# Optimization experiments

Hardware: AMD Instinct MI355X
Metric: run time of the kernel (lower is better)

Reference implementation:

```python
import jax, jax.numpy as jnp
import numpy as np

N = 100000
E = 1600000
IN_C = 64
HID = 32
HEADS = 4
OUT_C = 1
NEG_SLOPE = 0.2
BN_EPS = 1e-5


def setup_inputs() -> dict:
    key = jax.random.key(0)
    ks = jax.random.split(key, 12)
    x = jax.random.normal(ks[0], (N, IN_C), dtype=jnp.float32)
    edge_index = jax.random.randint(ks[1], (2, E), 0, N, dtype=jnp.int32)
    # GATConv layer 1: in -> heads*hid, concat=True
    W1 = jax.random.normal(ks[2], (IN_C, HEADS * HID), dtype=jnp.float32) * (1.0 / np.sqrt(IN_C))
    att_src1 = jax.random.normal(ks[3], (HEADS, HID), dtype=jnp.float32) * 0.1
    att_dst1 = jax.random.normal(ks[4], (HEADS, HID), dtype=jnp.float32) * 0.1
    b1 = jnp.zeros((HEADS * HID,), dtype=jnp.float32)
    # GATConv layer 2: heads*hid -> out, heads=1, concat=False
    W2 = jax.random.normal(ks[5], (HEADS * HID, OUT_C), dtype=jnp.float32) * (1.0 / np.sqrt(HEADS * HID))
    att_src2 = jax.random.normal(ks[6], (1, OUT_C), dtype=jnp.float32) * 0.1
    att_dst2 = jax.random.normal(ks[7], (1, OUT_C), dtype=jnp.float32) * 0.1
    b2 = jnp.zeros((OUT_C,), dtype=jnp.float32)
    # BatchNorm1d (eval mode, running stats)
    bn_gamma = jnp.ones((HEADS * HID,), dtype=jnp.float32)
    bn_beta = jnp.zeros((HEADS * HID,), dtype=jnp.float32)
    bn_mean = jnp.zeros((HEADS * HID,), dtype=jnp.float32)
    bn_var = jnp.ones((HEADS * HID,), dtype=jnp.float32)
    return {"x": x, "edge_index": edge_index, "W1": W1, "att_src1": att_src1,
            "att_dst1": att_dst1, "b1": b1, "W2": W2, "att_src2": att_src2,
            "att_dst2": att_dst2, "b2": b2, "bn_gamma": bn_gamma, "bn_beta": bn_beta,
            "bn_mean": bn_mean, "bn_var": bn_var}


def _gat_layer(x, src, dst, W, a_src, a_dst, heads, out_c, n):
    # linear transform, split heads: [N, heads, out_c]
    h = (x @ W).reshape(n, heads, out_c)
    # per-node attention terms: [N, heads]
    alpha_s = jnp.einsum('nhc,hc->nh', h, a_src)
    alpha_d = jnp.einsum('nhc,hc->nh', h, a_dst)
    # edge logits: [E, heads]
    e = jax.nn.leaky_relu(alpha_s[src] + alpha_d[dst], NEG_SLOPE)
    # segment softmax over edges sharing a destination node
    e_max = jax.ops.segment_max(e, dst, num_segments=n)
    e = jnp.exp(e - e_max[dst])
    denom = jax.ops.segment_sum(e, dst, num_segments=n)
    alpha = e / (denom[dst] + 1e-16)                 # [E, heads]
    msg = h[src] * alpha[:, :, None]                 # [E, heads, out_c]
    return jax.ops.segment_sum(msg, dst, num_segments=n)  # [N, heads, out_c]


def reference(x, edge_index, W1, att_src1, att_dst1, b1, W2, att_src2, att_dst2,
              b2, bn_gamma, bn_beta, bn_mean, bn_var):
    n = x.shape[0]
    loops = jnp.arange(n, dtype=edge_index.dtype)
    src = jnp.concatenate([edge_index[0], loops])    # PyG GATConv adds self-loops
    dst = jnp.concatenate([edge_index[1], loops])
    # layer 1: concat heads
    h = _gat_layer(x, src, dst, W1, att_src1, att_dst1, HEADS, HID, n)
    h = h.reshape(n, HEADS * HID) + b1
    # BatchNorm1d (eval) + ELU (dropout is identity in eval)
    h = (h - bn_mean) * jax.lax.rsqrt(bn_var + BN_EPS) * bn_gamma + bn_beta
    h = jax.nn.elu(h)
    # layer 2: single head, concat=False (mean over 1 head == squeeze)
    out = _gat_layer(h, src, dst, W2, att_src2, att_dst2, 1, OUT_C, n)
    return out.reshape(n, OUT_C) + b2
```

## Files before the change

### kernel.cpp

```cpp
#include <hip/hip_runtime.h>
#include <cstdint>
#include <cstddef>

#define NEG_SLOPE 0.2f
#define BN_EPS 1e-5f
#define BK_SHIFT 8
#define MAXBK 512
#define CHUNK 2048
#define CAP 8192

typedef _Float16 half4 __attribute__((ext_vector_type(4)));

__global__ void prep_kernel(const float* __restrict__ b1,
                            const float* __restrict__ bn_gamma,
                            const float* __restrict__ bn_beta,
                            const float* __restrict__ bn_mean,
                            const float* __restrict__ bn_var,
                            float* __restrict__ pre0,
                            float* __restrict__ pre1,
                            int* __restrict__ bucket_cursor) {
    int t = threadIdx.x;
    if (t < 128) {
        float sc = rsqrtf(bn_var[t] + BN_EPS) * bn_gamma[t];
        pre0[t] = sc;
        pre1[t] = (b1[t] - bn_mean[t]) * sc + bn_beta[t];
    }
    if (t < MAXBK) bucket_cursor[t] = 0;
}

__global__ void gemm1_kernel(const float* __restrict__ x,
                             const float* __restrict__ W1,
                             const float* __restrict__ att_s,
                             const float* __restrict__ att_d,
                             _Float16* __restrict__ h0,
                             float* __restrict__ as1,
                             float* __restrict__ ad1,
                             int N) {
    int c = threadIdx.x & 127;
    int pair = __builtin_amdgcn_readfirstlane(threadIdx.x >> 7);
    int n0 = (blockIdx.x * 2 + pair) * 4;
    if (n0 >= N) return;
    float acc[4] = {0.f, 0.f, 0.f, 0.f};
    const float* __restrict__ xr = x + (size_t)n0 * 64;
    int nn = N - n0; if (nn > 4) nn = 4;
    if (nn == 4) {
#pragma unroll
        for (int k = 0; k < 64; ++k) {
            float w = W1[k * 128 + c];
            acc[0] = fmaf(xr[k],       w, acc[0]);
            acc[1] = fmaf(xr[64 + k],  w, acc[1]);
            acc[2] = fmaf(xr[128 + k], w, acc[2]);
            acc[3] = fmaf(xr[192 + k], w, acc[3]);
        }
    } else {
        for (int i = 0; i < nn; ++i)
            for (int k = 0; k < 64; ++k)
                acc[i] = fmaf(xr[i * 64 + k], W1[k * 128 + c], acc[i]);
    }
    float asc = att_s[c], adc = att_d[c];
    int head = c >> 5;
#pragma unroll
    for (int i = 0; i < 4; ++i) {
        if (i >= nn) break;
        int n = n0 + i;
        h0[(size_t)n * 128 + c] = (_Float16)acc[i];
        float s = acc[i] * asc;
        float d = acc[i] * adc;
#pragma unroll
        for (int off = 16; off >= 1; off >>= 1) {
            s += __shfl_xor(s, off);
            d += __shfl_xor(d, off);
        }
        if ((threadIdx.x & 31) == 0) {
            as1[(size_t)n * 4 + head] = s;
            ad1[(size_t)n * 4 + head] = d;
        }
    }
}

__global__ void bin_kernel(const int* __restrict__ ei, int E, int N, int NBK,
                           int* __restrict__ bucket_cursor,
                           unsigned int* __restrict__ binned) {
    __shared__ int cnt[MAXBK];
    __shared__ int gstart[MAXBK];
    __shared__ int cur[MAXBK];
    int T = E + N;
    for (int b = threadIdx.x; b < NBK; b += 256) { cnt[b] = 0; cur[b] = 0; }
    __syncthreads();
    int base = blockIdx.x * CHUNK;
#pragma unroll
    for (int k = 0; k < CHUNK; k += 256) {
        int i = base + k + threadIdx.x;
        if (i < T) {
            int dst = (i < E) ? ei[E + i] : (i - E);
            atomicAdd(&cnt[dst >> BK_SHIFT], 1);
        }
    }
    __syncthreads();
    for (int b = threadIdx.x; b < NBK; b += 256) {
        int c = cnt[b];
        if (c) gstart[b] = atomicAdd(&bucket_cursor[b], c);
    }
    __syncthreads();
#pragma unroll
    for (int k = 0; k < CHUNK; k += 256) {
        int i = base + k + threadIdx.x;
        if (i < T) {
            int src, dst;
            if (i < E) { src = ei[i]; dst = ei[E + i]; }
            else       { src = i - E; dst = src; }
            int b = dst >> BK_SHIFT;
            int lp = gstart[b] + atomicAdd(&cur[b], 1);
            if (lp < CAP)
                binned[(size_t)b * CAP + lp] =
                    (unsigned int)src | ((unsigned int)(dst & 255) << 24);
        }
    }
}

__global__ void csr_kernel(const unsigned int* __restrict__ binned,
                           const int* __restrict__ bucket_cursor,
                           int N,
                           int* __restrict__ row_beg,
                           int* __restrict__ row_end,
                           int* __restrict__ csr_src) {
    __shared__ int cnt[256];
    __shared__ int loc[256];
    __shared__ int cur[256];
    int b = blockIdx.x;
    int tid = threadIdx.x;
    int n0 = b << BK_SHIFT;
    int nr = N - n0; if (nr > 256) nr = 256;
    int tot = bucket_cursor[b];
    if (tot > CAP) tot = CAP;
    size_t base = (size_t)b * CAP;
    cnt[tid] = 0;
    __syncthreads();
    for (int j = tid; j < tot; j += 256) {
        atomicAdd(&cnt[binned[base + j] >> 24], 1);
    }
    __syncthreads();
    int v = cnt[tid];
    loc[tid] = v;
    __syncthreads();
    for (int off = 1; off < 256; off <<= 1) {
        int t = (tid >= off) ? loc[tid - off] : 0;
        __syncthreads();
        loc[tid] += t;
        __syncthreads();
    }
    int excl = loc[tid] - v;
    cur[tid] = excl;
    if (tid < nr) {
        row_beg[n0 + tid] = (int)base + excl;
        row_end[n0 + tid] = (int)base + excl + v;
    }
    __syncthreads();
    for (int j = tid; j < tot; j += 256) {
        unsigned int w = binned[base + j];
        int pos = atomicAdd(&cur[w >> 24], 1);
        csr_src[base + pos] = (int)(w & 0xFFFFFFu);
    }
}

__global__ void gather1_kernel(const int* __restrict__ row_beg,
                               const int* __restrict__ row_end,
                               const int* __restrict__ csr_src,
                               const half4* __restrict__ h0,
                               const float* __restrict__ as1,
                               const float* __restrict__ ad1,
                               const float* __restrict__ pre0,
                               const float* __restrict__ pre1,
                               const float* __restrict__ W2,
                               float* __restrict__ h2, int N) {
    int n = blockIdx.x * 4 + (threadIdx.x >> 6);
    if (n >= N) return;
    int lane = threadIdx.x & 63;
    int sub  = lane & 31;
    int grp  = lane >> 5;
    int head = sub >> 3;
    float ad = ad1[(size_t)n * 4 + head];
    int beg = row_beg[n];
    int end = row_end[n];
    float4 acc = make_float4(0.f, 0.f, 0.f, 0.f);
    float den = 0.f;
#pragma unroll 2
    for (int j = beg + grp; j < end; j += 2) {
        int src = csr_src[j];
        float as = as1[(size_t)src * 4 + head];
        float lg = as + ad;
        float l = fmaf(NEG_SLOPE, fminf(lg, 0.f), fmaxf(lg, 0.f));
        float w = __expf(l);
        half4 hv = h0[(size_t)src * 32 + sub];
        acc.x = fmaf(w, (float)hv.x, acc.x);
        acc.y = fmaf(w, (float)hv.y, acc.y);
        acc.z = fmaf(w, (float)hv.z, acc.z);
        acc.w = fmaf(w, (float)hv.w, acc.w);
        den += w;
    }
    acc.x += __shfl_xor(acc.x, 32);
    acc.y += __shfl_xor(acc.y, 32);
    acc.z += __shfl_xor(acc.z, 32);
    acc.w += __shfl_xor(acc.w, 32);
    den   += __shfl_xor(den, 32);
    float inv = 1.f / (den + 1e-16f);
    int c = sub * 4;
    float v0 = fmaf(acc.x * inv, pre0[c],     pre1[c]);
    float v1 = fmaf(acc.y * inv, pre0[c + 1], pre1[c + 1]);
    float v2 = fmaf(acc.z * inv, pre0[c + 2], pre1[c + 2]);
    float v3 = fmaf(acc.w * inv, pre0[c + 3], pre1[c + 3]);
    v0 = v0 > 0.f ? v0 : expm1f(v0);
    v1 = v1 > 0.f ? v1 : expm1f(v1);
    v2 = v2 > 0.f ? v2 : expm1f(v2);
    v3 = v3 > 0.f ? v3 : expm1f(v3);
    float t = v0 * W2[c] + v1 * W2[c + 1] + v2 * W2[c + 2] + v3 * W2[c + 3];
#pragma unroll
    for (int off = 16; off >= 1; off >>= 1) t += __shfl_xor(t, off);
    if (lane == 0) h2[n] = t;
}

__global__ void gather2_kernel(const int* __restrict__ row_beg,
                               const int* __restrict__ row_end,
                               const int* __restrict__ csr_src,
                               const float* __restrict__ h2,
                               const float* __restrict__ att_s2,
                               const float* __restrict__ att_d2,
                               const float* __restrict__ b2,
                               float* __restrict__ out, int N) {
    int n = blockIdx.x * 16 + (threadIdx.x >> 4);
    if (n >= N) return;
    int lane = threadIdx.x & 15;
    int beg = row_beg[n];
    int end = row_end[n];
    float a_s = att_s2[0];
    float a_d = att_d2[0];
    float hd = h2[n];
    float num = 0.f, den = 0.f;
    for (int j = beg + lane; j < end; j += 16) {
        int src = csr_src[j];
        float hs = h2[src];
        float lg = hs * a_s + hd * a_d;
        float l = fmaf(NEG_SLOPE, fminf(lg, 0.f), fmaxf(lg, 0.f));
        float w = __expf(l);
        num += w * hs;
        den += w;
    }
#pragma unroll
    for (int off = 8; off >= 1; off >>= 1) {
        num += __shfl_xor(num, off);
        den += __shfl_xor(den, off);
    }
    if (lane == 0) out[n] = num / (den + 1e-16f) + b2[0];
}

extern "C" void kernel_launch(void* const* d_in, const int* in_sizes, int n_in,
                              void* d_out, int out_size, void* d_ws, size_t ws_size,
                              hipStream_t stream) {
    const float* x     = (const float*)d_in[0];
    const int*   ei    = (const int*)  d_in[1];
    const float* W1    = (const float*)d_in[2];
    const float* atts1 = (const float*)d_in[3];
    const float* attd1 = (const float*)d_in[4];
    const float* b1    = (const float*)d_in[5];
    const float* W2    = (const float*)d_in[6];
    const float* atts2 = (const float*)d_in[7];
    const float* attd2 = (const float*)d_in[8];
    const float* b2    = (const float*)d_in[9];
    const float* bn_g  = (const float*)d_in[10];
    const float* bn_b  = (const float*)d_in[11];
    const float* bn_m  = (const float*)d_in[12];
    const float* bn_v  = (const float*)d_in[13];

    const int N = in_sizes[0] / 64;
    const int E = in_sizes[1] / 2;
    const int T = E + N;
    const int NBK = (N + 255) >> BK_SHIFT;
    const int NCH = (T + CHUNK - 1) / CHUNK;

    char* p = (char*)d_ws;
    auto alloc = [&](size_t bytes, size_t align) -> void* {
        uintptr_t q = ((uintptr_t)p + align - 1) & ~(uintptr_t)(align - 1);
        p = (char*)(q + bytes);
        return (void*)q;
    };
    _Float16* h0      = (_Float16*)alloc((size_t)N * 128 * 2, 16);
    float* as1        = (float*)alloc((size_t)N * 4 * 4, 16);
    float* ad1        = (float*)alloc((size_t)N * 4 * 4, 16);
    float* h2         = (float*)alloc((size_t)N * 4, 16);
    float* pre0       = (float*)alloc(128 * 4, 16);
    float* pre1       = (float*)alloc(128 * 4, 16);
    int*   row_beg    = (int*)alloc((size_t)N * 4, 16);
    int*   row_end    = (int*)alloc((size_t)N * 4, 16);
    int*   bucket_cur = (int*)alloc((size_t)MAXBK * 4, 16);
    unsigned int* binned = (unsigned int*)alloc((size_t)NBK * CAP * 4, 16);
    int*   csr_src    = (int*)alloc((size_t)NBK * CAP * 4, 16);

    prep_kernel<<<1, 512, 0, stream>>>(b1, bn_g, bn_b, bn_m, bn_v,
                                       pre0, pre1, bucket_cur);

    bin_kernel<<<NCH, 256, 0, stream>>>(ei, E, N, NBK, bucket_cur, binned);
    csr_kernel<<<NBK, 256, 0, stream>>>(binned, bucket_cur, N,
                                        row_beg, row_end, csr_src);

    gemm1_kernel<<<(N + 7) / 8, 256, 0, stream>>>(
        x, W1, atts1, attd1, h0, as1, ad1, N);

    gather1_kernel<<<(N + 3) / 4, 256, 0, stream>>>(
        row_beg, row_end, csr_src, (const half4*)h0, as1, ad1, pre0, pre1,
        W2, h2, N);

    gather2_kernel<<<(N + 15) / 16, 256, 0, stream>>>(
        row_beg, row_end, csr_src, h2, atts2, attd2, b2, (float*)d_out, N);
}
```

Before: 311.3 us.

## Fuse edge binning with GEMM launch and stage attention weights in gather1

Merges the edge-binning kernel and the layer-1 GEMM into one launch that splits blocks by index, so the two independent stages can run concurrently and one launch is removed. CHUNK grows so fewer binning blocks issue fewer global cursor atomics, though each block does more serial work. gather1 now computes the per-edge, per-head attention weights once per 16-edge batch into shared memory instead of redundantly in every lane, then reuses them for the feature gather. The shared-memory staging relies on wave-level lockstep with no barrier, and edge order within a bucket is now nondeterministic across concurrent blocks, as before.

Measured after the change: 284.8 us. 8.5% less time.

```diff
diff --git a/kernel.cpp b/kernel.cpp
--- a/kernel.cpp
+++ b/kernel.cpp
@@ -6,7 +6,7 @@
 #define BN_EPS 1e-5f
 #define BK_SHIFT 8
 #define MAXBK 512
-#define CHUNK 2048
+#define CHUNK 8192
 #define CAP 8192
 
 typedef _Float16 half4 __attribute__((ext_vector_type(4)));
@@ -28,17 +28,59 @@
     if (t < MAXBK) bucket_cursor[t] = 0;
 }
 
-__global__ void gemm1_kernel(const float* __restrict__ x,
-                             const float* __restrict__ W1,
-                             const float* __restrict__ att_s,
-                             const float* __restrict__ att_d,
-                             _Float16* __restrict__ h0,
-                             float* __restrict__ as1,
-                             float* __restrict__ ad1,
-                             int N) {
+__global__ void gemm_bin_kernel(
+                                const float* __restrict__ x,
+                                const float* __restrict__ W1,
+                                const float* __restrict__ att_s,
+                                const float* __restrict__ att_d,
+                                _Float16* __restrict__ h0,
+                                float* __restrict__ as1,
+                                float* __restrict__ ad1,
+                                int N,
+                                const int* __restrict__ ei, int E, int NBK,
+                                int* __restrict__ bucket_cursor,
+                                unsigned int* __restrict__ binned,
+                                int NCH) {
+    __shared__ int cnt[MAXBK];
+    __shared__ int gstart[MAXBK];
+    __shared__ int cur[MAXBK];
+    if (blockIdx.x < NCH) {
+        int T = E + N;
+        for (int b = threadIdx.x; b < NBK; b += 256) { cnt[b] = 0; cur[b] = 0; }
+        __syncthreads();
+        int base = blockIdx.x * CHUNK;
+        for (int k = 0; k < CHUNK; k += 256) {
+            int i = base + k + threadIdx.x;
+            if (i < T) {
+                int dst = (i < E) ? ei[E + i] : (i - E);
+                atomicAdd(&cnt[dst >> BK_SHIFT], 1);
+            }
+        }
+        __syncthreads();
+        for (int b = threadIdx.x; b < NBK; b += 256) {
+            int c = cnt[b];
+            if (c) gstart[b] = atomicAdd(&bucket_cursor[b], c);
+        }
+        __syncthreads();
+        for (int k = 0; k < CHUNK; k += 256) {
+            int i = base + k + threadIdx.x;
+            if (i < T) {
+                int src, dst;
+                if (i < E) { src = ei[i]; dst = ei[E + i]; }
+                else       { src = i - E; dst = src; }
+                int b = dst >> BK_SHIFT;
+                int lp = gstart[b] + atomicAdd(&cur[b], 1);
+                if (lp < CAP)
+                    binned[(size_t)b * CAP + lp] =
+                        (unsigned int)src | ((unsigned int)(dst & 255) << 24);
+            }
+        }
+        return;
+    }
+    int bid = blockIdx.x - NCH;
     int c = threadIdx.x & 127;
     int pair = __builtin_amdgcn_readfirstlane(threadIdx.x >> 7);
-    int n0 = (blockIdx.x * 2 + pair) * 4;
+    int n0 = (bid * 2 + pair) * 4;
     if (n0 >= N) return;
     float acc[4] = {0.f, 0.f, 0.f, 0.f};
     const float* __restrict__ xr = x + (size_t)n0 * 64;
@@ -74,46 +116,6 @@
         if ((threadIdx.x & 31) == 0) {
             as1[(size_t)n * 4 + head] = s;
             ad1[(size_t)n * 4 + head] = d;
-        }
-    }
-}
-
-__global__ void bin_kernel(const int* __restrict__ ei, int E, int N, int NBK,
-                           int* __restrict__ bucket_cursor,
-                           unsigned int* __restrict__ binned) {
-    __shared__ int cnt[MAXBK];
-    __shared__ int gstart[MAXBK];
-    __shared__ int cur[MAXBK];
-    int T = E + N;
-    for (int b = threadIdx.x; b < NBK; b += 256) { cnt[b] = 0; cur[b] = 0; }
-    __syncthreads();
-    int base = blockIdx.x * CHUNK;
-#pragma unroll
-    for (int k = 0; k < CHUNK; k += 256) {
-        int i = base + k + threadIdx.x;
-        if (i < T) {
-            int dst = (i < E) ? ei[E + i] : (i - E);
-            atomicAdd(&cnt[dst >> BK_SHIFT], 1);
-        }
-    }
-    __syncthreads();
-    for (int b = threadIdx.x; b < NBK; b += 256) {
-        int c = cnt[b];
-        if (c) gstart[b] = atomicAdd(&bucket_cursor[b], c);
-    }
-    __syncthreads();
-#pragma unroll
-    for (int k = 0; k < CHUNK; k += 256) {
-        int i = base + k + threadIdx.x;
-        if (i < T) {
-            int src, dst;
-            if (i < E) { src = ei[i]; dst = ei[E + i]; }
-            else       { src = i - E; dst = src; }
-            int b = dst >> BK_SHIFT;
-            int lp = gstart[b] + atomicAdd(&cur[b], 1);
-            if (lp < CAP)
-                binned[(size_t)b * CAP + lp] =
-                    (unsigned int)src | ((unsigned int)(dst & 255) << 24);
         }
     }
 }
@@ -173,42 +175,59 @@
                                const float* __restrict__ pre1,
                                const float* __restrict__ W2,
                                float* __restrict__ h2, int N) {
-    int n = blockIdx.x * 4 + (threadIdx.x >> 6);
+    __shared__ int   s_src[4][16];
+    __shared__ float s_w[4][16][4];
+    int wv = threadIdx.x >> 6;
+    int n = blockIdx.x * 4 + wv;
     if (n >= N) return;
     int lane = threadIdx.x & 63;
-    int sub  = lane & 31;
-    int grp  = lane >> 5;
-    int head = sub >> 3;
-    float ad = ad1[(size_t)n * 4 + head];
+    int e1 = lane >> 2;
+    int h1 = lane & 3;
+    float ad_p1 = ad1[(size_t)n * 4 + h1];
+    int sub   = lane & 31;
+    int grp   = lane >> 5;
+    int head2 = sub >> 3;
     int beg = row_beg[n];
     int end = row_end[n];
     float4 acc = make_float4(0.f, 0.f, 0.f, 0.f);
-    float den = 0.f;
-#pragma unroll 2
-    for (int j = beg + grp; j < end; j += 2) {
-        int src = csr_src[j];
-        float as = as1[(size_t)src * 4 + head];
-        float lg = as + ad;
-        float l = fmaf(NEG_SLOPE, fminf(lg, 0.f), fmaxf(lg, 0.f));
-        float w = __expf(l);
-        half4 hv = h0[(size_t)src * 32 + sub];
-        acc.x = fmaf(w, (float)hv.x, acc.x);
-        acc.y = fmaf(w, (float)hv.y, acc.y);
-        acc.z = fmaf(w, (float)hv.z, acc.z);
-        acc.w = fmaf(w, (float)hv.w, acc.w);
-        den += w;
-    }
+    float denl = 0.f;
+    for (int jb = beg; jb < end; jb += 16) {
+        int cnt = end - jb; if (cnt > 16) cnt = 16;
+        if (e1 < cnt) {
+            int src = csr_src[jb + e1];
+            float as = as1[(size_t)src * 4 + h1];
+            float lg = as + ad_p1;
+            float l = fmaf(NEG_SLOPE, fminf(lg, 0.f), fmaxf(lg, 0.f));
+            float w = __expf(l);
+            s_w[wv][e1][h1] = w;
+            if (h1 == 0) s_src[wv][e1] = src;
+            denl += w;
+        }
+        for (int t = grp; t < cnt; t += 2) {
+            int src = s_src[wv][t];
+            float w = s_w[wv][t][head2];
+            half4 hv = h0[(size_t)src * 32 + sub];
+            acc.x = fmaf(w, (float)hv.x, acc.x);
+            acc.y = fmaf(w, (float)hv.y, acc.y);
+            acc.z = fmaf(w, (float)hv.z, acc.z);
+            acc.w = fmaf(w, (float)hv.w, acc.w);
+        }
+    }
+    denl += __shfl_xor(denl, 4);
+    denl += __shfl_xor(denl, 8);
+    denl += __shfl_xor(denl, 16);
+    denl += __shfl_xor(denl, 32);
+    float inv = 1.f / (denl + 1e-16f);
+    float invv = __shfl(inv, head2);
     acc.x += __shfl_xor(acc.x, 32);
     acc.y += __shfl_xor(acc.y, 32);
     acc.z += __shfl_xor(acc.z, 32);
     acc.w += __shfl_xor(acc.w, 32);
-    den   += __shfl_xor(den, 32);
-    float inv = 1.f / (den + 1e-16f);
     int c = sub * 4;
-    float v0 = fmaf(acc.x * inv, pre0[c],     pre1[c]);
-    float v1 = fmaf(acc.y * inv, pre0[c + 1], pre1[c + 1]);
-    float v2 = fmaf(acc.z * inv, pre0[c + 2], pre1[c + 2]);
-    float v3 = fmaf(acc.w * inv, pre0[c + 3], pre1[c + 3]);
+    float v0 = fmaf(acc.x * invv, pre0[c],     pre1[c]);
+    float v1 = fmaf(acc.y * invv, pre0[c + 1], pre1[c + 1]);
+    float v2 = fmaf(acc.z * invv, pre0[c + 2], pre1[c + 2]);
+    float v3 = fmaf(acc.w * invv, pre0[c + 3], pre1[c + 3]);
     v0 = v0 > 0.f ? v0 : expm1f(v0);
     v1 = v1 > 0.f ? v1 : expm1f(v1);
     v2 = v2 > 0.f ? v2 : expm1f(v2);
@@ -276,6 +295,7 @@
     const int T = E + N;
     const int NBK = (N + 255) >> BK_SHIFT;
     const int NCH = (T + CHUNK - 1) / CHUNK;
+    const int NGB = (N + 7) / 8;
 
     char* p = (char*)d_ws;
     auto alloc = [&](size_t bytes, size_t align) -> void* {
@@ -298,12 +318,12 @@
     prep_kernel<<<1, 512, 0, stream>>>(b1, bn_g, bn_b, bn_m, bn_v,
                                        pre0, pre1, bucket_cur);
 
-    bin_kernel<<<NCH, 256, 0, stream>>>(ei, E, N, NBK, bucket_cur, binned);
+    gemm_bin_kernel<<<NCH + NGB, 256, 0, stream>>>(
+        x, W1, atts1, attd1, h0, as1, ad1, N,
+        ei, E, NBK, bucket_cur, binned, NCH);
+
     csr_kernel<<<NBK, 256, 0, stream>>>(binned, bucket_cur, N,
                                         row_beg, row_end, csr_src);
-
-    gemm1_kernel<<<(N + 7) / 8, 256, 0, stream>>>(
-        x, W1, atts1, attd1, h0, as1, ad1, N);
 
     gather1_kernel<<<(N + 3) / 4, 256, 0, stream>>>(
         row_beg, row_end, csr_src, (const half4*)h0, as1, ad1, pre0, pre1,
```
